# Kernel tuning notes

Hardware: AMD Instinct MI355X
Metric: run time of the kernel (lower is better)

The kernel has to match this reference:

```python
import jax, jax.numpy as jnp
import numpy as np

D_MODEL = 768
N_HEADS = 12
D_FF = 3072
EPS = 1e-5


def _layernorm(x, g, b):
    mu = jnp.mean(x, axis=-1, keepdims=True)
    var = jnp.mean(jnp.square(x - mu), axis=-1, keepdims=True)
    return (x - mu) * jax.lax.rsqrt(var + EPS) * g + b


def setup_inputs() -> dict:
    key = jax.random.key(0)
    ks = jax.random.split(key, 16)
    d, f = D_MODEL, D_FF
    s = 1.0 / np.sqrt(d)
    inp = {
        "x": jax.random.normal(ks[0], (1, 4096, d), dtype=jnp.float32),
        "Wq": jax.random.normal(ks[1], (d, d), dtype=jnp.float32) * s,
        "bq": jnp.zeros((d,), jnp.float32),
        "Wk": jax.random.normal(ks[2], (d, d), dtype=jnp.float32) * s,
        "bk": jnp.zeros((d,), jnp.float32),
        "Wv": jax.random.normal(ks[3], (d, d), dtype=jnp.float32) * s,
        "bv": jnp.zeros((d,), jnp.float32),
        "Wo": jax.random.normal(ks[4], (d, d), dtype=jnp.float32) * s,
        "bo": jnp.zeros((d,), jnp.float32),
        "ln1_g": jnp.ones((d,), jnp.float32),
        "ln1_b": jnp.zeros((d,), jnp.float32),
        "ln2_g": jnp.ones((d,), jnp.float32),
        "ln2_b": jnp.zeros((d,), jnp.float32),
        "W1": jax.random.normal(ks[5], (d, f), dtype=jnp.float32) * s,
        "b1": jnp.zeros((f,), jnp.float32),
        "W2": jax.random.normal(ks[6], (f, d), dtype=jnp.float32) * (1.0 / np.sqrt(f)),
        "b2": jnp.zeros((d,), jnp.float32),
    }
    return inp


def reference(x, Wq, bq, Wk, bk, Wv, bv, Wo, bo, ln1_g, ln1_b, ln2_g, ln2_b, W1, b1, W2, b2):
    b, s, d = x.shape
    h = N_HEADS
    dk = d // h

    # --- attention sublayer (pre-norm residual) ---
    xn = _layernorm(x, ln1_g, ln1_b)

    def proj(W, bias):
        y = xn @ W + bias                      # [b, s, d]
        return y.reshape(b, s, h, dk).transpose(0, 2, 1, 3)  # [b, h, s, dk]

    q, k, v = proj(Wq, bq), proj(Wk, bk), proj(Wv, bv)
    scores = jnp.einsum("bhqd,bhkd->bhqk", q, k) / np.sqrt(dk)
    attn = jax.nn.softmax(scores, axis=-1)
    ctx = jnp.einsum("bhqk,bhkd->bhqd", attn, v)
    ctx = ctx.transpose(0, 2, 1, 3).reshape(b, s, d)
    x = x + (ctx @ Wo + bo)

    # --- FFN sublayer (pre-norm residual) ---
    xn2 = _layernorm(x, ln2_g, ln2_b)
    ff = jax.nn.gelu(xn2 @ W1 + b1, approximate=False) @ W2 + b2
    return x + ff
```

## Files before the change

### kernel.cpp

```cpp
#include <hip/hip_runtime.h>
#include <hip/hip_bf16.h>

typedef __attribute__((ext_vector_type(8))) __bf16 bf16x8;
typedef __attribute__((ext_vector_type(4))) __bf16 bf16x4;
typedef __attribute__((ext_vector_type(4))) float f32x4;
typedef __attribute__((ext_vector_type(4))) unsigned short u16x4;
typedef __attribute__((ext_vector_type(8))) unsigned short u16x8;
typedef unsigned short ushort_t;

__device__ __forceinline__ ushort_t f2bf(float f) {
    union { float f; unsigned u; } v; v.f = f;
    unsigned r = v.u + 0x7fffu + ((v.u >> 16) & 1u);
    return (ushort_t)(r >> 16);
}

__device__ __forceinline__ void gload16(const ushort_t* g, ushort_t* l) {
    __builtin_amdgcn_global_load_lds(
        (const __attribute__((address_space(1))) unsigned int*)g,
        (__attribute__((address_space(3))) unsigned int*)l,
        16, 0, 0);
}

__device__ __forceinline__ void ln_row(const float* __restrict__ xr,
                                       const float* __restrict__ g,
                                       const float* __restrict__ b,
                                       ushort_t* __restrict__ orow, int t) {
    float v0 = xr[t], v1 = xr[t + 256], v2 = xr[t + 512];
    float s  = v0 + v1 + v2;
    float s2 = v0 * v0 + v1 * v1 + v2 * v2;
#pragma unroll
    for (int off = 32; off; off >>= 1) {
        s  += __shfl_down(s, off);
        s2 += __shfl_down(s2, off);
    }
    __shared__ float red[8];
    const int wid = t >> 6, lane = t & 63;
    if (lane == 0) { red[wid] = s; red[4 + wid] = s2; }
    __syncthreads();
    __shared__ float stats[2];
    if (t == 0) {
        float S = red[0] + red[1] + red[2] + red[3];
        float S2 = red[4] + red[5] + red[6] + red[7];
        float mu = S * (1.0f / 768.0f);
        float var = S2 * (1.0f / 768.0f) - mu * mu;
        stats[0] = mu;
        stats[1] = rsqrtf(var + 1e-5f);
    }
    __syncthreads();
    const float mu = stats[0], rs = stats[1];
    orow[t]       = f2bf((v0 - mu) * rs * g[t]       + b[t]);
    orow[t + 256] = f2bf((v1 - mu) * rs * g[t + 256] + b[t + 256]);
    orow[t + 512] = f2bf((v2 - mu) * rs * g[t + 512] + b[t + 512]);
}

__global__ __launch_bounds__(256) void ln_kernel(const float* __restrict__ x,
                                                 const float* __restrict__ g,
                                                 const float* __restrict__ b,
                                                 ushort_t* __restrict__ out) {
    const int row = blockIdx.x;
    ln_row(x + (size_t)row * 768, g, b, out + (size_t)row * 768, threadIdx.x);
}

__global__ __launch_bounds__(256) void prep_ln(
    const float* __restrict__ Wq, const float* __restrict__ Wk,
    const float* __restrict__ Wv, const float* __restrict__ Wo,
    const float* __restrict__ W1, const float* __restrict__ W2,
    const float* __restrict__ bq, const float* __restrict__ bk,
    const float* __restrict__ bv,
    const float* __restrict__ x, const float* __restrict__ ln1_g,
    const float* __restrict__ ln1_b,
    ushort_t* __restrict__ WqkvT, ushort_t* __restrict__ WoT,
    ushort_t* __restrict__ W1T, ushort_t* __restrict__ W2T,
    float* __restrict__ bqkv, ushort_t* __restrict__ xn) {
    const int bid = blockIdx.x;
    const int t = threadIdx.x;
    if (bid >= 6915) {
        const int row = bid - 6915;
        ln_row(x + (size_t)row * 768, ln1_g, ln1_b, xn + (size_t)row * 768, t);
        return;
    }
    if (bid >= 6912) {
        const int i = bid - 6912;
        const float* s = (i == 0) ? bq : (i == 1) ? bk : bv;
#pragma unroll
        for (int j = t; j < 768; j += 256) bqkv[i * 768 + j] = s[j];
        return;
    }
    const float* src; ushort_t* dst; int R, C, ti;
    if (bid < 576)       { src = Wq; dst = WqkvT;               R = 768;  C = 768;  ti = bid; }
    else if (bid < 1152) { src = Wk; dst = WqkvT + 768 * 768;   R = 768;  C = 768;  ti = bid - 576; }
    else if (bid < 1728) { src = Wv; dst = WqkvT + 2 * 768 * 768; R = 768; C = 768; ti = bid - 1152; }
    else if (bid < 2304) { src = Wo; dst = WoT;                 R = 768;  C = 768;  ti = bid - 1728; }
    else if (bid < 4608) { src = W1; dst = W1T;                 R = 768;  C = 3072; ti = bid - 2304; }
    else                 { src = W2; dst = W2T;                 R = 3072; C = 768;  ti = bid - 4608; }
    const int tpr = C >> 5;
    const int c0 = (ti % tpr) * 32, r0 = (ti / tpr) * 32;
    __shared__ float tile[32][33];
    {
        const int c = t & 31, r = t >> 5;
#pragma unroll
        for (int i = 0; i < 4; i++)
            tile[r + i * 8][c] = src[(size_t)(r0 + r + i * 8) * C + c0 + c];
    }
    __syncthreads();
    {
        const int oc = t >> 3, q = t & 7;
        u16x4 o;
#pragma unroll
        for (int k = 0; k < 4; k++) o[k] = f2bf(tile[q * 4 + k][oc]);
        *(u16x4*)&dst[(size_t)(c0 + oc) * R + r0 + q * 4] = o;
    }
}

template <int BN, int GELU, int RES, int OUTF, int OUTB, int OUTV>
__global__ __launch_bounds__(256, 3)
void gemm_bt(const ushort_t* __restrict__ A, const ushort_t* __restrict__ Bt,
             const float* __restrict__ bias, const float* __restrict__ res,
             float* __restrict__ outF, ushort_t* __restrict__ outB, int ldo,
             ushort_t* __restrict__ outV,
             int M, int N, int K) {
    constexpr int TR  = 128 + BN;
    constexpr int LL  = TR / 64;
    constexpr int WCF = BN / 32;
    __shared__ __align__(16) ushort_t Ls[2][TR * 32];

    const int nbx = gridDim.x;
    const int nwg = nbx * gridDim.y;
    int fb = blockIdx.y * nbx + blockIdx.x;
    fb = (fb & 7) * (nwg >> 3) + (fb >> 3);
    const int m0 = (fb / nbx) * 128, n0 = (fb % nbx) * BN;

    const int t = threadIdx.x;
    const int wid = t >> 6, lane = t & 63;
    const int wr = wid >> 1, wc = wid & 1;
    const int row16 = lane & 15, kg = lane >> 4;
    const int kb = kg * 8;

    const int srow = lane >> 2, scol = (lane & 3) * 8;
    const ushort_t* gsrc[LL];
    int lofs[LL];
#pragma unroll
    for (int i = 0; i < LL; i++) {
        const int r0 = wid * (TR / 4) + 16 * i;
        gsrc[i] = (r0 < 128 ? A + (size_t)(m0 + r0 + srow) * K
                            : Bt + (size_t)(n0 + r0 - 128 + srow) * K) + scol;
        lofs[i] = r0 * 32;
    }

#define STAGE(buf, kofs) do {                                        \
        _Pragma("unroll")                                            \
        for (int i = 0; i < LL; i++)                                 \
            gload16(gsrc[i] + (kofs), &Ls[buf][lofs[i]]);            \
    } while (0)

    f32x4 acc[4][WCF] = {};
    const int NS = K >> 5;
    STAGE(0, 0);
    STAGE(1, 32);
    int cur = 0;

    for (int s = 0; s < NS; ++s) {
        if (s + 1 == NS) asm volatile("s_waitcnt vmcnt(0)" ::: "memory");
        else             asm volatile("s_waitcnt vmcnt(%0)" :: "i"(LL) : "memory");
        __builtin_amdgcn_s_barrier();

        bf16x8 a[4], b[WCF];
#pragma unroll
        for (int i = 0; i < 4; i++)
            a[i] = *(const bf16x8*)&Ls[cur][(wr * 64 + i * 16 + row16) * 32 + kb];
#pragma unroll
        for (int j = 0; j < WCF; j++)
            b[j] = *(const bf16x8*)&Ls[cur][(128 + wc * (BN / 2) + j * 16 + row16) * 32 + kb];
        asm volatile("s_waitcnt lgkmcnt(0)" ::: "memory");
        __builtin_amdgcn_s_barrier();
        if (s + 2 < NS) STAGE(cur, (s + 2) * 32);

        __builtin_amdgcn_s_setprio(1);
#pragma unroll
        for (int i = 0; i < 4; i++)
#pragma unroll
            for (int j = 0; j < WCF; j++)
                acc[i][j] = __builtin_amdgcn_mfma_f32_16x16x32_bf16(a[i], b[j], acc[i][j], 0, 0, 0);
        __builtin_amdgcn_s_setprio(0);
        cur ^= 1;
    }
#undef STAGE

#pragma unroll
    for (int i = 0; i < 4; i++)
#pragma unroll
        for (int j = 0; j < WCF; j++) {
            const int col = n0 + wc * (BN / 2) + j * 16 + row16;
            const float bv = bias[col];
            const int rb = m0 + wr * 64 + i * 16 + kg * 4;
            if (OUTV && col >= 1536) {
                bf16x4 pk;
#pragma unroll
                for (int r = 0; r < 4; r++) pk[r] = (__bf16)(acc[i][j][r] + bv);
                *(bf16x4*)&outV[(size_t)(col - 1536) * 4096 + rb] = pk;
            } else {
#pragma unroll
                for (int r = 0; r < 4; r++) {
                    const int row = rb + r;
                    float v = acc[i][j][r] + bv;
                    if (GELU) {
                        float u = v + 0.044715f * v * v * v;
                        float e = __builtin_amdgcn_exp2f(2.30220779f * u);
                        v = v * e * __builtin_amdgcn_rcpf(e + 1.0f);
                    }
                    if (RES) v += res[(size_t)row * N + col];
                    if (OUTF) outF[(size_t)row * N + col] = v;
                    if (OUTB) outB[(size_t)row * ldo + col] = f2bf(v);
                }
            }
        }
}

__device__ __forceinline__ int swz(int row, int col) {
    return row * 64 + (col ^ ((row & 7) << 3));
}

__global__ __launch_bounds__(256, 3)
void attn_kernel(const ushort_t* __restrict__ qk,
                 const ushort_t* __restrict__ Vt,
                 ushort_t* __restrict__ num0, ushort_t* __restrict__ num1,
                 float* __restrict__ den) {
    int fb = blockIdx.y * 32 + blockIdx.x;
    fb = (fb & 7) * 96 + (fb >> 3);
    const int q0 = (fb & 31) * 128;
    const int hs = fb >> 5;
    const int h = hs >> 1, sp = hs & 1;
    const int kt0 = sp * 32;

    const int t  = threadIdx.x;
    const int w = t >> 6, lane = t & 63;
    const int row16 = lane & 15, kg = lane >> 4;
    const int kb = kg * 8;

    __shared__ __align__(16) ushort_t Ps[128 * 64];
    __shared__ __align__(16) ushort_t Ks[2][64 * 64];
    __shared__ __align__(16) ushort_t Vs[2][64 * 64];

    {
        const int qr = t >> 1, cb = (t & 1) * 32;
        const size_t qbase = (size_t)(q0 + qr) * 1536 + h * 64 + cb;
#pragma unroll
        for (int j = 0; j < 4; j++)
            *(uint4*)&Ps[swz(qr, cb + j * 8)] = *(const uint4*)&qk[qbase + j * 8];
    }
    {
        const int sr = t >> 2, sc = (t & 3) * 8;
        const size_t kbase = (size_t)(kt0 * 64 + sr) * 1536 + 768 + h * 64 + sc;
        *(uint4*)&Ks[0][swz(sr, sc)]      = *(const uint4*)&qk[kbase];
        *(uint4*)&Ks[0][swz(sr, sc + 32)] = *(const uint4*)&qk[kbase + 32];
        const size_t vbase = (size_t)(h * 64 + sr) * 4096 + kt0 * 64 + sc;
        *(uint4*)&Vs[0][swz(sr, sc)]      = *(const uint4*)&Vt[vbase];
        *(uint4*)&Vs[0][swz(sr, sc + 32)] = *(const uint4*)&Vt[vbase + 32];
    }
    bf16x8 qa0[2], qa1[2];
#pragma unroll
    for (int qb = 0; qb < 2; qb++) {
        qa0[qb] = *(const bf16x8*)&Ps[swz(w * 32 + qb * 16 + row16, kb)];
        qa1[qb] = *(const bf16x8*)&Ps[swz(w * 32 + qb * 16 + row16, 32 + kb)];
    }
    __syncthreads();

    const int rr = lane >> 3;
    const int gcol = ((lane & 7) ^ rr) * 8;
    const ushort_t* gK = qk + 768 + h * 64 + gcol + (size_t)(w * 16 + rr) * 1536;
    const ushort_t* gV = Vt + (size_t)(h * 64 + w * 16 + rr) * 4096 + gcol;

    bf16x8 vones;
#pragma unroll
    for (int i = 0; i < 8; i++) vones[i] = (__bf16)1.0f;

    f32x4 o_acc[2][4] = {};
    f32x4 o_l[2] = {};
    int cur = 0;
    const float SC = 0.18033688011112042f;

    for (int it = 0; it < 32; ++it) {
        if (it != 31) {
            const int kv1 = (kt0 + it + 1) * 64;
            ushort_t* kd = &Ks[cur ^ 1][w * 1024];
            ushort_t* vd = &Vs[cur ^ 1][w * 1024];
            gload16(gK + (size_t)kv1 * 1536,       kd);
            gload16(gK + (size_t)(kv1 + 8) * 1536, kd + 512);
            gload16(gV + kv1,                      vd);
            gload16(gV + kv1 + 8 * 4096,           vd + 512);
        }

        const ushort_t* Kc = Ks[cur];
        const ushort_t* Vc = Vs[cur];

        bf16x8 ka0[4], ka1[4];
#pragma unroll
        for (int f = 0; f < 4; f++) {
            ka0[f] = *(const bf16x8*)&Kc[swz(f * 16 + row16, kb)];
            ka1[f] = *(const bf16x8*)&Kc[swz(f * 16 + row16, 32 + kb)];
        }

        f32x4 s_acc[2][4];
        __builtin_amdgcn_s_setprio(1);
#pragma unroll
        for (int qb = 0; qb < 2; qb++)
#pragma unroll
            for (int f = 0; f < 4; f++) {
                f32x4 z = {};
                z = __builtin_amdgcn_mfma_f32_16x16x32_bf16(ka0[f], qa0[qb], z, 0, 0, 0);
                s_acc[qb][f] = __builtin_amdgcn_mfma_f32_16x16x32_bf16(ka1[f], qa1[qb], z, 0, 0, 0);
            }
        __builtin_amdgcn_s_setprio(0);

#pragma unroll
        for (int qb = 0; qb < 2; qb++)
#pragma unroll
            for (int f = 0; f < 4; f++) {
                bf16x4 pk;
#pragma unroll
                for (int r = 0; r < 4; r++)
                    pk[r] = (__bf16)__builtin_amdgcn_exp2f(fminf(s_acc[qb][f][r] * SC, 30.0f));
                *(bf16x4*)&Ps[swz(w * 32 + qb * 16 + row16, f * 16 + kg * 4)] = pk;
            }

        bf16x8 pa0[2], pa1[2];
#pragma unroll
        for (int qb = 0; qb < 2; qb++) {
            pa0[qb] = *(const bf16x8*)&Ps[swz(w * 32 + qb * 16 + row16, kb)];
            pa1[qb] = *(const bf16x8*)&Ps[swz(w * 32 + qb * 16 + row16, 32 + kb)];
        }
        __builtin_amdgcn_s_setprio(1);
#pragma unroll
        for (int f = 0; f < 4; f++) {
            bf16x8 vb0 = *(const bf16x8*)&Vc[swz(f * 16 + row16, kb)];
            bf16x8 vb1 = *(const bf16x8*)&Vc[swz(f * 16 + row16, 32 + kb)];
#pragma unroll
            for (int qb = 0; qb < 2; qb++) {
                o_acc[qb][f] = __builtin_amdgcn_mfma_f32_16x16x32_bf16(pa0[qb], vb0, o_acc[qb][f], 0, 0, 0);
                o_acc[qb][f] = __builtin_amdgcn_mfma_f32_16x16x32_bf16(pa1[qb], vb1, o_acc[qb][f], 0, 0, 0);
            }
        }
#pragma unroll
        for (int qb = 0; qb < 2; qb++) {
            o_l[qb] = __builtin_amdgcn_mfma_f32_16x16x32_bf16(pa0[qb], vones, o_l[qb], 0, 0, 0);
            o_l[qb] = __builtin_amdgcn_mfma_f32_16x16x32_bf16(pa1[qb], vones, o_l[qb], 0, 0, 0);
        }
        __builtin_amdgcn_s_setprio(0);

        __syncthreads();
        cur ^= 1;
    }

    ushort_t* np = sp ? num1 : num0;
#pragma unroll
    for (int qb = 0; qb < 2; qb++)
#pragma unroll
        for (int f = 0; f < 4; f++)
#pragma unroll
            for (int r = 0; r < 4; r++) {
                const int qrow = q0 + w * 32 + qb * 16 + kg * 4 + r;
                np[(size_t)qrow * 768 + h * 64 + f * 16 + row16] = f2bf(o_acc[qb][f][r]);
            }
    if (row16 == 0) {
#pragma unroll
        for (int qb = 0; qb < 2; qb++)
#pragma unroll
            for (int r = 0; r < 4; r++) {
                const int qrow = q0 + w * 32 + qb * 16 + kg * 4 + r;
                den[((size_t)sp * 12 + h) * 4096 + qrow] = o_l[qb][r];
            }
    }
}

__global__ __launch_bounds__(256) void attn_combine(
    const ushort_t* __restrict__ num0, const ushort_t* __restrict__ num1,
    const float* __restrict__ den, ushort_t* __restrict__ ctx) {
    const int idx = blockIdx.x * 256 + threadIdx.x;
    const int q = idx / 96;
    const int g = idx % 96;
    const int h = g >> 3;
    const float rd = __builtin_amdgcn_rcpf(den[(size_t)h * 4096 + q] +
                                           den[((size_t)12 + h) * 4096 + q]);
    const size_t o = (size_t)q * 768 + g * 8;
    u16x8 a = *(const u16x8*)&num0[o];
    u16x8 b = *(const u16x8*)&num1[o];
    u16x8 pk;
#pragma unroll
    for (int i = 0; i < 8; i++) {
        const float av = __uint_as_float((unsigned)a[i] << 16);
        const float bv = __uint_as_float((unsigned)b[i] << 16);
        pk[i] = f2bf((av + bv) * rd);
    }
    *(u16x8*)&ctx[o] = pk;
}

extern "C" void kernel_launch(void* const* d_in, const int* in_sizes, int n_in,
                              void* d_out, int out_size, void* d_ws, size_t ws_size,
                              hipStream_t stream) {
    const float* x     = (const float*)d_in[0];
    const float* Wq    = (const float*)d_in[1];
    const float* bq    = (const float*)d_in[2];
    const float* Wk    = (const float*)d_in[3];
    const float* bk    = (const float*)d_in[4];
    const float* Wv    = (const float*)d_in[5];
    const float* bv    = (const float*)d_in[6];
    const float* Wo    = (const float*)d_in[7];
    const float* bo    = (const float*)d_in[8];
    const float* ln1_g = (const float*)d_in[9];
    const float* ln1_b = (const float*)d_in[10];
    const float* ln2_g = (const float*)d_in[11];
    const float* ln2_b = (const float*)d_in[12];
    const float* W1    = (const float*)d_in[13];
    const float* b1    = (const float*)d_in[14];
    const float* W2    = (const float*)d_in[15];
    const float* b2    = (const float*)d_in[16];

    char* ws = (char*)d_ws;
    ushort_t* WqkvT = (ushort_t*)ws; ws += (size_t)2304 * 768 * 2;
    ushort_t* WoT   = (ushort_t*)ws; ws += (size_t)768 * 768 * 2;
    ushort_t* W1T   = (ushort_t*)ws; ws += (size_t)3072 * 768 * 2;
    ushort_t* W2T   = (ushort_t*)ws; ws += (size_t)768 * 3072 * 2;
    float*    bqkv  = (float*)ws;    ws += (size_t)2304 * 4;
    ushort_t* xn    = (ushort_t*)ws; ws += (size_t)4096 * 768 * 2;
    ushort_t* qk    = (ushort_t*)ws; ws += (size_t)4096 * 1536 * 2;
    ushort_t* Vtb   = (ushort_t*)ws; ws += (size_t)768 * 4096 * 2;
    ushort_t* ctxb  = (ushort_t*)ws; ws += (size_t)4096 * 768 * 2;
    float*    x1    = (float*)ws;    ws += (size_t)4096 * 768 * 4;
    ushort_t* num0b = (ushort_t*)ws; ws += (size_t)4096 * 768 * 2;
    ushort_t* num1b = (ushort_t*)ws; ws += (size_t)4096 * 768 * 2;
    float*    den   = (float*)ws;    ws += (size_t)2 * 12 * 4096 * 4;
    ushort_t* H     = qk;

    prep_ln<<<6915 + 4096, 256, 0, stream>>>(Wq, Wk, Wv, Wo, W1, W2, bq, bk, bv,
                                             x, ln1_g, ln1_b,
                                             WqkvT, WoT, W1T, W2T, bqkv, xn);

    gemm_bt<128, 0, 0, 0, 1, 1><<<dim3(18, 32), 256, 0, stream>>>(
        xn, WqkvT, bqkv, nullptr, nullptr, qk, 1536, Vtb, 4096, 2304, 768);

    attn_kernel<<<dim3(32, 24), 256, 0, stream>>>(qk, Vtb, num0b, num1b, den);
    attn_combine<<<1536, 256, 0, stream>>>(num0b, num1b, den, ctxb);

    gemm_bt<64, 0, 1, 1, 0, 0><<<dim3(12, 32), 256, 0, stream>>>(
        ctxb, WoT, bo, x, x1, nullptr, 0, nullptr, 4096, 768, 768);

    ln_kernel<<<4096, 256, 0, stream>>>(x1, ln2_g, ln2_b, xn);
    gemm_bt<128, 1, 0, 0, 1, 0><<<dim3(24, 32), 256, 0, stream>>>(
        xn, W1T, b1, nullptr, nullptr, H, 3072, nullptr, 4096, 3072, 768);
    gemm_bt<64, 0, 1, 1, 0, 0><<<dim3(12, 32), 256, 0, stream>>>(
        H, W2T, b2, x1, (float*)d_out, nullptr, 0, nullptr, 4096, 768, 3072);

    (void)in_sizes; (void)n_in; (void)out_size; (void)ws_size;
}
```

Before: 199.3 us.

## Add dedicated 128x64 GEMM kernel for N=768 outputs and fold softmax scale into Q

Adds a specialized gemm_bt64 kernel for the Wo and W2 projections, which produce a 768-wide output. It uses a unified 192-row LDS tile, double-buffered global-to-LDS loads with explicit vmcnt waits, and occupancy of 3 blocks per CU. Separately, the softmax scale is multiplied into Q in the QKV GEMM epilogue, so the attention inner loop no longer does a multiply per score. The Q values are rounded to bf16 after scaling, which slightly changes their rounding.

```diff
diff --git a/kernel.cpp b/kernel.cpp
--- a/kernel.cpp
+++ b/kernel.cpp
@@ -208,10 +208,102 @@
                         float e = __builtin_amdgcn_exp2f(2.30220779f * u);
                         v = v * e * __builtin_amdgcn_rcpf(e + 1.0f);
                     }
+                    if (OUTV && col < 768) v *= 0.18033688011112042f;
                     if (RES) v += res[(size_t)row * N + col];
                     if (OUTF) outF[(size_t)row * N + col] = v;
                     if (OUTB) outB[(size_t)row * ldo + col] = f2bf(v);
                 }
+            }
+        }
+}
+
+__global__ __launch_bounds__(256, 3)
+void gemm_bt64(const ushort_t* __restrict__ A, const ushort_t* __restrict__ Bt,
+               const float* __restrict__ bias, const float* __restrict__ res,
+               float* __restrict__ outF, int M, int N, int K) {
+    constexpr int TR = 192, BK = 64, LL = 6;
+    __shared__ __align__(16) ushort_t Ls[2][TR * BK];
+
+    const int nbx = gridDim.x;
+    const int nwg = nbx * gridDim.y;
+    int fb = blockIdx.y * nbx + blockIdx.x;
+    fb = (fb & 7) * (nwg >> 3) + (fb >> 3);
+    const int m0 = (fb / nbx) * 128, n0 = (fb % nbx) * 64;
+
+    const int t = threadIdx.x;
+    const int wid = t >> 6, lane = t & 63;
+    const int wr = wid >> 1, wc = wid & 1;
+    const int row16 = lane & 15, kg = lane >> 4;
+    const int rsw = row16 & 7;
+
+    const int srow = lane >> 3;
+    const int sslot = (lane & 7) ^ srow;
+    const ushort_t* gsrc[LL];
+    int lofs[LL];
+#pragma unroll
+    for (int i = 0; i < LL; i++) {
+        const int r0 = wid * 48 + 8 * i;
+        gsrc[i] = (r0 < 128 ? A + (size_t)(m0 + r0 + srow) * K
+                            : Bt + (size_t)(n0 + r0 - 128 + srow) * K) + sslot * 8;
+        lofs[i] = r0 * BK;
+    }
+
+#define STAGEP(buf, kofs) do {                                       \
+        _Pragma("unroll")                                            \
+        for (int i = 0; i < LL; i++)                                 \
+            gload16(gsrc[i] + (kofs), &Ls[buf][lofs[i]]);            \
+    } while (0)
+
+    f32x4 acc[4][2] = {};
+    const int NS = K >> 6;
+    STAGEP(0, 0);
+    STAGEP(1, BK);
+    int cur = 0;
+
+    for (int s = 0; s < NS; ++s) {
+        if (s + 1 == NS) asm volatile("s_waitcnt vmcnt(0)" ::: "memory");
+        else             asm volatile("s_waitcnt vmcnt(%0)" :: "i"(LL) : "memory");
+        __builtin_amdgcn_s_barrier();
+
+        bf16x8 a[2][4], b[2][2];
+#pragma unroll
+        for (int kk = 0; kk < 2; kk++) {
+            const int sA = ((kk * 4 + kg) ^ rsw) * 8;
+#pragma unroll
+            for (int i = 0; i < 4; i++)
+                a[kk][i] = *(const bf16x8*)&Ls[cur][(wr * 64 + i * 16 + row16) * BK + sA];
+#pragma unroll
+            for (int j = 0; j < 2; j++)
+                b[kk][j] = *(const bf16x8*)&Ls[cur][(128 + wc * 32 + j * 16 + row16) * BK + sA];
+        }
+        asm volatile("s_waitcnt lgkmcnt(0)" ::: "memory");
+        __builtin_amdgcn_s_barrier();
+        if (s + 2 < NS) STAGEP(cur, (s + 2) * BK);
+
+        __builtin_amdgcn_s_setprio(1);
+#pragma unroll
+        for (int kk = 0; kk < 2; kk++)
+#pragma unroll
+            for (int i = 0; i < 4; i++)
+#pragma unroll
+                for (int j = 0; j < 2; j++)
+                    acc[i][j] = __builtin_amdgcn_mfma_f32_16x16x32_bf16(a[kk][i], b[kk][j], acc[i][j], 0, 0, 0);
+        __builtin_amdgcn_s_setprio(0);
+        cur ^= 1;
+    }
+#undef STAGEP
+
+#pragma unroll
+    for (int i = 0; i < 4; i++)
+#pragma unroll
+        for (int j = 0; j < 2; j++) {
+            const int col = n0 + wc * 32 + j * 16 + row16;
+            const float bv = bias[col];
+            const int rb = m0 + wr * 64 + i * 16 + kg * 4;
+#pragma unroll
+            for (int r = 0; r < 4; r++) {
+                const int row = rb + r;
+                outF[(size_t)row * N + col] = acc[i][j][r] + bv + res[(size_t)row * N + col];
             }
         }
 }
@@ -277,7 +369,6 @@
     f32x4 o_acc[2][4] = {};
     f32x4 o_l[2] = {};
     int cur = 0;
-    const float SC = 0.18033688011112042f;
 
     for (int it = 0; it < 32; ++it) {
         if (it != 31) {
@@ -319,7 +410,7 @@
                 bf16x4 pk;
 #pragma unroll
                 for (int r = 0; r < 4; r++)
-                    pk[r] = (__bf16)__builtin_amdgcn_exp2f(fminf(s_acc[qb][f][r] * SC, 30.0f));
+                    pk[r] = (__bf16)__builtin_amdgcn_exp2f(fminf(s_acc[qb][f][r], 30.0f));
                 *(bf16x4*)&Ps[swz(w * 32 + qb * 16 + row16, f * 16 + kg * 4)] = pk;
             }
 
@@ -441,14 +532,14 @@
     attn_kernel<<<dim3(32, 24), 256, 0, stream>>>(qk, Vtb, num0b, num1b, den);
     attn_combine<<<1536, 256, 0, stream>>>(num0b, num1b, den, ctxb);
 
-    gemm_bt<64, 0, 1, 1, 0, 0><<<dim3(12, 32), 256, 0, stream>>>(
-        ctxb, WoT, bo, x, x1, nullptr, 0, nullptr, 4096, 768, 768);
+    gemm_bt64<<<dim3(12, 32), 256, 0, stream>>>(ctxb, WoT, bo, x, x1,
+                                                4096, 768, 768);
 
     ln_kernel<<<4096, 256, 0, stream>>>(x1, ln2_g, ln2_b, xn);
     gemm_bt<128, 1, 0, 0, 1, 0><<<dim3(24, 32), 256, 0, stream>>>(
         xn, W1T, b1, nullptr, nullptr, H, 3072, nullptr, 4096, 3072, 768);
-    gemm_bt<64, 0, 1, 1, 0, 0><<<dim3(12, 32), 256, 0, stream>>>(
-        H, W2T, b2, x1, (float*)d_out, nullptr, 0, nullptr, 4096, 768, 3072);
+    gemm_bt64<<<dim3(12, 32), 256, 0, stream>>>(H, W2T, b2, x1, (float*)d_out,
+                                                4096, 768, 3072);
 
     (void)in_sizes; (void)n_in; (void)out_size; (void)ws_size;
 }
```

Result: faster. 194.4 us (-2.4%).

## Use single 128x64 GEMM with BK=64 XOR-swizzled LDS; fold attention scale into Q

Applied to the files above, without the earlier changes.

Replaces the templated GEMM with one 128x64 tile kernel that stages K=64 per step into an XOR-swizzled LDS layout. Each barrier pair now covers two MFMA k-steps, which halves the number of sync rounds and should avoid LDS bank conflicts. The QKV and FFN1 GEMMs move from 128-wide to 64-wide N tiles, so the grids are twice as large and the A tile is reloaded more often. The softmax scale is applied to Q in the QKV epilogue, which removes a multiply per score inside attention. This adds one bf16 rounding of the scaled Q.

```diff
diff --git a/kernel.cpp b/kernel.cpp
--- a/kernel.cpp
+++ b/kernel.cpp
@@ -112,51 +112,50 @@
     }
 }
 
-template <int BN, int GELU, int RES, int OUTF, int OUTB, int OUTV>
+template <int GELU, int RES, int OUTF, int OUTB, int OUTV>
 __global__ __launch_bounds__(256, 3)
-void gemm_bt(const ushort_t* __restrict__ A, const ushort_t* __restrict__ Bt,
-             const float* __restrict__ bias, const float* __restrict__ res,
-             float* __restrict__ outF, ushort_t* __restrict__ outB, int ldo,
-             ushort_t* __restrict__ outV,
-             int M, int N, int K) {
-    constexpr int TR  = 128 + BN;
-    constexpr int LL  = TR / 64;
-    constexpr int WCF = BN / 32;
-    __shared__ __align__(16) ushort_t Ls[2][TR * 32];
+void gemm64(const ushort_t* __restrict__ A, const ushort_t* __restrict__ Bt,
+            const float* __restrict__ bias, const float* __restrict__ res,
+            float* __restrict__ outF, ushort_t* __restrict__ outB, int ldo,
+            ushort_t* __restrict__ outV,
+            int M, int N, int K) {
+    constexpr int TR = 192, BK = 64, LL = 6;
+    __shared__ __align__(16) ushort_t Ls[2][TR * BK];
 
     const int nbx = gridDim.x;
     const int nwg = nbx * gridDim.y;
     int fb = blockIdx.y * nbx + blockIdx.x;
     fb = (fb & 7) * (nwg >> 3) + (fb >> 3);
-    const int m0 = (fb / nbx) * 128, n0 = (fb % nbx) * BN;
+    const int m0 = (fb / nbx) * 128, n0 = (fb % nbx) * 64;
 
     const int t = threadIdx.x;
     const int wid = t >> 6, lane = t & 63;
     const int wr = wid >> 1, wc = wid & 1;
     const int row16 = lane & 15, kg = lane >> 4;
-    const int kb = kg * 8;
-
-    const int srow = lane >> 2, scol = (lane & 3) * 8;
+    const int rsw = row16 & 7;
+
+    const int srow = lane >> 3;
+    const int sslot = (lane & 7) ^ srow;
     const ushort_t* gsrc[LL];
     int lofs[LL];
 #pragma unroll
     for (int i = 0; i < LL; i++) {
-        const int r0 = wid * (TR / 4) + 16 * i;
+        const int r0 = wid * 48 + 8 * i;
         gsrc[i] = (r0 < 128 ? A + (size_t)(m0 + r0 + srow) * K
-                            : Bt + (size_t)(n0 + r0 - 128 + srow) * K) + scol;
-        lofs[i] = r0 * 32;
-    }
-
-#define STAGE(buf, kofs) do {                                        \
+                            : Bt + (size_t)(n0 + r0 - 128 + srow) * K) + sslot * 8;
+        lofs[i] = r0 * BK;
+    }
+
+#define STAGEP(buf, kofs) do {                                       \
         _Pragma("unroll")                                            \
         for (int i = 0; i < LL; i++)                                 \
             gload16(gsrc[i] + (kofs), &Ls[buf][lofs[i]]);            \
     } while (0)
 
-    f32x4 acc[4][WCF] = {};
-    const int NS = K >> 5;
-    STAGE(0, 0);
-    STAGE(1, 32);
+    f32x4 acc[4][2] = {};
+    const int NS = K >> 6;
+    STAGEP(0, 0);
+    STAGEP(1, BK);
     int cur = 0;
 
     for (int s = 0; s < NS; ++s) {
@@ -164,33 +163,39 @@
         else             asm volatile("s_waitcnt vmcnt(%0)" :: "i"(LL) : "memory");
         __builtin_amdgcn_s_barrier();
 
-        bf16x8 a[4], b[WCF];
-#pragma unroll
-        for (int i = 0; i < 4; i++)
-            a[i] = *(const bf16x8*)&Ls[cur][(wr * 64 + i * 16 + row16) * 32 + kb];
-#pragma unroll
-        for (int j = 0; j < WCF; j++)
-            b[j] = *(const bf16x8*)&Ls[cur][(128 + wc * (BN / 2) + j * 16 + row16) * 32 + kb];
+        bf16x8 a[2][4], b[2][2];
+#pragma unroll
+        for (int kk = 0; kk < 2; kk++) {
+            const int sA = ((kk * 4 + kg) ^ rsw) * 8;
+#pragma unroll
+            for (int i = 0; i < 4; i++)
+                a[kk][i] = *(const bf16x8*)&Ls[cur][(wr * 64 + i * 16 + row16) * BK + sA];
+#pragma unroll
+            for (int j = 0; j < 2; j++)
+                b[kk][j] = *(const bf16x8*)&Ls[cur][(128 + wc * 32 + j * 16 + row16) * BK + sA];
+        }
         asm volatile("s_waitcnt lgkmcnt(0)" ::: "memory");
         __builtin_amdgcn_s_barrier();
-        if (s + 2 < NS) STAGE(cur, (s + 2) * 32);
+        if (s + 2 < NS) STAGEP(cur, (s + 2) * BK);
 
         __builtin_amdgcn_s_setprio(1);
 #pragma unroll
-        for (int i = 0; i < 4; i++)
-#pragma unroll
-            for (int j = 0; j < WCF; j++)
-                acc[i][j] = __builtin_amdgcn_mfma_f32_16x16x32_bf16(a[i], b[j], acc[i][j], 0, 0, 0);
+        for (int kk = 0; kk < 2; kk++)
+#pragma unroll
+            for (int i = 0; i < 4; i++)
+#pragma unroll
+                for (int j = 0; j < 2; j++)
+                    acc[i][j] = __builtin_amdgcn_mfma_f32_16x16x32_bf16(a[kk][i], b[kk][j], acc[i][j], 0, 0, 0);
         __builtin_amdgcn_s_setprio(0);
         cur ^= 1;
     }
-#undef STAGE
+#undef STAGEP
 
 #pragma unroll
     for (int i = 0; i < 4; i++)
 #pragma unroll
-        for (int j = 0; j < WCF; j++) {
-            const int col = n0 + wc * (BN / 2) + j * 16 + row16;
+        for (int j = 0; j < 2; j++) {
+            const int col = n0 + wc * 32 + j * 16 + row16;
             const float bv = bias[col];
             const int rb = m0 + wr * 64 + i * 16 + kg * 4;
             if (OUTV && col >= 1536) {
@@ -208,6 +213,7 @@
                         float e = __builtin_amdgcn_exp2f(2.30220779f * u);
                         v = v * e * __builtin_amdgcn_rcpf(e + 1.0f);
                     }
+                    if (OUTV && col < 768) v *= 0.18033688011112042f;
                     if (RES) v += res[(size_t)row * N + col];
                     if (OUTF) outF[(size_t)row * N + col] = v;
                     if (OUTB) outB[(size_t)row * ldo + col] = f2bf(v);
@@ -277,7 +283,6 @@
     f32x4 o_acc[2][4] = {};
     f32x4 o_l[2] = {};
     int cur = 0;
-    const float SC = 0.18033688011112042f;
 
     for (int it = 0; it < 32; ++it) {
         if (it != 31) {
@@ -319,7 +324,7 @@
                 bf16x4 pk;
 #pragma unroll
                 for (int r = 0; r < 4; r++)
-                    pk[r] = (__bf16)__builtin_amdgcn_exp2f(fminf(s_acc[qb][f][r] * SC, 30.0f));
+                    pk[r] = (__bf16)__builtin_amdgcn_exp2f(fminf(s_acc[qb][f][r], 30.0f));
                 *(bf16x4*)&Ps[swz(w * 32 + qb * 16 + row16, f * 16 + kg * 4)] = pk;
             }
 
@@ -435,19 +440,19 @@
                                              x, ln1_g, ln1_b,
                                              WqkvT, WoT, W1T, W2T, bqkv, xn);
 
-    gemm_bt<128, 0, 0, 0, 1, 1><<<dim3(18, 32), 256, 0, stream>>>(
+    gemm64<0, 0, 0, 1, 1><<<dim3(36, 32), 256, 0, stream>>>(
         xn, WqkvT, bqkv, nullptr, nullptr, qk, 1536, Vtb, 4096, 2304, 768);
 
     attn_kernel<<<dim3(32, 24), 256, 0, stream>>>(qk, Vtb, num0b, num1b, den);
     attn_combine<<<1536, 256, 0, stream>>>(num0b, num1b, den, ctxb);
 
-    gemm_bt<64, 0, 1, 1, 0, 0><<<dim3(12, 32), 256, 0, stream>>>(
+    gemm64<0, 1, 1, 0, 0><<<dim3(12, 32), 256, 0, stream>>>(
         ctxb, WoT, bo, x, x1, nullptr, 0, nullptr, 4096, 768, 768);
 
     ln_kernel<<<4096, 256, 0, stream>>>(x1, ln2_g, ln2_b, xn);
-    gemm_bt<128, 1, 0, 0, 1, 0><<<dim3(24, 32), 256, 0, stream>>>(
+    gemm64<1, 0, 0, 1, 0><<<dim3(48, 32), 256, 0, stream>>>(
         xn, W1T, b1, nullptr, nullptr, H, 3072, nullptr, 4096, 3072, 768);
-    gemm_bt<64, 0, 1, 1, 0, 0><<<dim3(12, 32), 256, 0, stream>>>(
+    gemm64<0, 1, 1, 0, 0><<<dim3(12, 32), 256, 0, stream>>>(
         H, W2T, b2, x1, (float*)d_out, nullptr, 0, nullptr, 4096, 768, 3072);
 
     (void)in_sizes; (void)n_in; (void)out_size; (void)ws_size;
```

Result: faster. 190.1 us (-4.6%).
